# Kernel optimization log

Hardware: AMD Instinct MI355X
Metric: run time of the kernel (lower is better)

The kernel has to match this reference:

```python
import jax, jax.numpy as jnp
import numpy as np

HEADS = 8
DIM_HEAD = 32
HTK = 576
WTK = 576


def layernorm(x, g, b, eps=1e-6):
    mu = x.mean(-1, keepdims=True)
    var = ((x - mu) ** 2).mean(-1, keepdims=True)
    return (x - mu) * jax.lax.rsqrt(var + eps) * g + b


def conv2d(x, w, b, pad, groups=1):
    y = jax.lax.conv_general_dilated(
        x, w, (1, 1), [(pad, pad), (pad, pad)],
        dimension_numbers=('NCHW', 'OIHW', 'NCHW'),
        feature_group_count=groups)
    return y + b[None, :, None, None]


def prune_attn(attn, htk, wtk):
    B, H, N, _ = attn.shape
    bi = jnp.arange(B)[:, None, None]
    hi = jnp.arange(H)[None, :, None]
    # row pruning: score rows by mean over keys, keep top-k rows
    row_scores = attn.mean(-1)                       # [B,H,N]
    _, top_row = jax.lax.top_k(row_scores, htk)      # [B,H,htk]
    row_mask = jnp.zeros((B, H, N), attn.dtype).at[bi, hi, top_row].set(1.0)
    # col pruning: score cols by mean over queries, keep top-k cols
    col_scores = attn.mean(-2)                       # [B,H,N]
    _, top_col = jax.lax.top_k(col_scores, wtk)
    col_mask = jnp.zeros((B, H, N), attn.dtype).at[bi, hi, top_col].set(1.0)
    return attn * row_mask[..., :, None] * col_mask[..., None, :]


def setup_inputs() -> dict:
    key = jax.random.key(0)
    ks = jax.random.split(key, 24)
    C = 256
    hid = C * 4
    g = C // 8
    s = 0.02
    inp = {
        'x': jax.random.normal(ks[0], (2, C, 48, 48), jnp.float32),
        'qkv_w': jax.random.normal(ks[1], (C, 3 * C), jnp.float32) * s,
        'out_w': jax.random.normal(ks[2], (C, C), jnp.float32) * s,
        'ln1_g': jnp.ones((C,), jnp.float32),
        'ln1_b': jnp.zeros((C,), jnp.float32),
        'ln2_g': jnp.ones((C,), jnp.float32),
        'ln2_b': jnp.zeros((C,), jnp.float32),
        'dw_w': jax.random.normal(ks[3], (C, 1, 3, 3), jnp.float32) * s,
        'dw_b': jnp.zeros((C,), jnp.float32),
        'pw_w': jax.random.normal(ks[4], (C, C, 1, 1), jnp.float32) * s,
        'pw_b': jnp.zeros((C,), jnp.float32),
        'sg1_w': jax.random.normal(ks[5], (g, C, 1, 1), jnp.float32) * s,
        'sg1_b': jnp.zeros((g,), jnp.float32),
        'sg2_w': jax.random.normal(ks[6], (1, g, 7, 7), jnp.float32) * s,
        'sg2_b': jnp.zeros((1,), jnp.float32),
        'cg1_w': jax.random.normal(ks[7], (g, C, 1, 1), jnp.float32) * s,
        'cg1_b': jnp.zeros((g,), jnp.float32),
        'cg2_w': jax.random.normal(ks[8], (C, g, 1, 1), jnp.float32) * s,
        'cg2_b': jnp.zeros((C,), jnp.float32),
        'ff_w1': jax.random.normal(ks[9], (C, hid), jnp.float32) * s,
        'ff_b1': jnp.zeros((hid,), jnp.float32),
        'ff_w2': jax.random.normal(ks[10], (hid, C), jnp.float32) * s,
        'ff_b2': jnp.zeros((C,), jnp.float32),
        'gamma1': jnp.full((1,), 0.5, jnp.float32),
        'gamma2': jnp.full((1,), 0.5, jnp.float32),
    }
    return inp


def reference(x, qkv_w, out_w, ln1_g, ln1_b, ln2_g, ln2_b, dw_w, dw_b,
              pw_w, pw_b, sg1_w, sg1_b, sg2_w, sg2_b, cg1_w, cg1_b,
              cg2_w, cg2_b, ff_w1, ff_b1, ff_w2, ff_b2, gamma1, gamma2):
    B, C, H, W = x.shape
    N = H * W
    # ---- dual-pruned self-attention branch ----
    xa = x.transpose(0, 2, 3, 1).reshape(B, N, C)
    xa = layernorm(xa, ln1_g, ln1_b)
    qkv = xa @ qkv_w                                    # [B,N,3C]
    q, k, v = jnp.split(qkv, 3, axis=-1)
    rs = lambda t: t.reshape(B, N, HEADS, DIM_HEAD).transpose(0, 2, 1, 3)
    q, k, v = rs(q), rs(k), rs(v)                       # [B,h,N,d]
    attn = jnp.einsum('bhid,bhjd->bhij', q, k) * (DIM_HEAD ** -0.5)
    attn = prune_attn(attn, HTK, WTK)
    attn = jax.nn.softmax(attn, axis=-1)
    o = jnp.einsum('bhij,bhjd->bhid', attn, v)
    o = o.transpose(0, 2, 1, 3).reshape(B, N, C) @ out_w
    x_attn = o.reshape(B, H, W, C).transpose(0, 3, 1, 2)
    # ---- conv branch ----
    xc = conv2d(x, dw_w, dw_b, pad=1, groups=C)
    xc = conv2d(xc, pw_w, pw_b, pad=0)
    xs = x_attn + xc
    # ---- gates ----
    sg = jax.nn.silu(conv2d(xs, sg1_w, sg1_b, pad=0))
    sg = jax.nn.sigmoid(conv2d(sg, sg2_w, sg2_b, pad=3))   # [B,1,H,W]
    cg = xs.mean(axis=(2, 3), keepdims=True)                # [B,C,1,1]
    cg = jax.nn.silu(conv2d(cg, cg1_w, cg1_b, pad=0))
    cg = jax.nn.sigmoid(conv2d(cg, cg2_w, cg2_b, pad=0))
    x2 = x + gamma1[0] * (xs * sg * cg)
    # ---- FFN ----
    normed = layernorm(x2.transpose(0, 2, 3, 1), ln2_g, ln2_b)
    h = jax.nn.gelu(normed @ ff_w1 + ff_b1, approximate=False)
    ff = (h @ ff_w2 + ff_b2).transpose(0, 3, 1, 2)
    return x2 + gamma2[0] * ff
```

## Files before the change

kernel.cpp:

```cpp
#include <hip/hip_runtime.h>
#include <math.h>

#define N_PIX 2304
#define CCH   256
#define BHN   16
#define KTOP  576
#define NROWS 4608

typedef unsigned short u16;
typedef __attribute__((ext_vector_type(8))) short short8v;
typedef __attribute__((ext_vector_type(4))) float floatx4;

__device__ __forceinline__ u16 f2b(float f) {
  unsigned int u = __float_as_uint(f);
  return (u16)((u + 0x7fffu + ((u >> 16) & 1u)) >> 16);
}
__device__ __forceinline__ float b2f(u16 v) {
  return __uint_as_float(((unsigned int)v) << 16);
}

__device__ __forceinline__ void async16(const void* g, void* l) {
  __builtin_amdgcn_global_load_lds(
      (const __attribute__((address_space(1))) unsigned int*)g,
      (__attribute__((address_space(3))) unsigned int*)l, 16, 0, 0);
}

__global__ __launch_bounds__(256) void ln1t_kernel(
    const float* __restrict__ x, u16* __restrict__ xa_bf, float* __restrict__ xnhwc,
    const float* __restrict__ g, const float* __restrict__ beta)
{
  __shared__ float tile[32 * 257];
  __shared__ float redS[8 * 32], redQ[8 * 32];
  __shared__ float mu_s[32], rs_s[32];
  int tid = threadIdx.x;
  int p0g = blockIdx.x * 32;
  int bb = p0g / N_PIX; int p0 = p0g - bb * N_PIX;
  int px = tid & 31, csub = tid >> 5;
  float sacc = 0.f, qacc = 0.f;
#pragma unroll 4
  for (int it = 0; it < 32; ++it) {
    int c = it * 8 + csub;
    float v = x[((long)bb * 256 + c) * N_PIX + p0 + px];
    tile[px * 257 + c] = v;
    sacc += v; qacc += v * v;
  }
  redS[csub * 32 + px] = sacc; redQ[csub * 32 + px] = qacc;
  __syncthreads();
  if (tid < 32) {
    float s = 0.f, qq = 0.f;
#pragma unroll
    for (int j = 0; j < 8; ++j) { s += redS[j * 32 + tid]; qq += redQ[j * 32 + tid]; }
    float mu = s * (1.f / 256.f);
    float var = qq * (1.f / 256.f) - mu * mu;
    mu_s[tid] = mu; rs_s[tid] = rsqrtf(var + 1e-6f);
  }
  __syncthreads();
  float gv = g[tid], bv = beta[tid];
#pragma unroll 4
  for (int it = 0; it < 32; ++it) {
    float v = tile[it * 257 + tid];
    long orow = (long)(p0g + it) * 256 + tid;
    xnhwc[orow] = v;
    xa_bf[orow] = f2b((v - mu_s[it]) * rs_s[it] * gv + bv);
  }
}

__global__ __launch_bounds__(256) void cast_all_kernel(
    const float* __restrict__ qkv_w, const float* __restrict__ out_w,
    const float* __restrict__ pw_w, const float* __restrict__ ff_w1,
    const float* __restrict__ ff_w2, const float* __restrict__ sg1_w,
    u16* __restrict__ qkvBT, u16* __restrict__ outBT, u16* __restrict__ pwBT,
    u16* __restrict__ ff1BT, u16* __restrict__ ff2BT, u16* __restrict__ sg1BT)
{
  int i = blockIdx.x * 256 + threadIdx.x;
  if (i < 196608) { int k = i / 768, n = i - k * 768; qkvBT[n * 256 + k] = f2b(qkv_w[i]); return; }
  i -= 196608;
  if (i < 65536) { int k = i >> 8, n = i & 255; outBT[n * 256 + k] = f2b(out_w[i]); return; }
  i -= 65536;
  if (i < 65536) { pwBT[i] = f2b(pw_w[i]); return; }
  i -= 65536;
  if (i < 262144) { int k = i >> 10, n = i & 1023; ff1BT[n * 256 + k] = f2b(ff_w1[i]); return; }
  i -= 262144;
  if (i < 262144) { int k = i & 1023, n = i >> 10; ff2BT[i] = f2b(ff_w2[k * 256 + n]); return; }
  i -= 262144;
  if (i < 16384) sg1BT[i] = (i < 8192) ? f2b(sg1_w[i]) : (u16)0;
}

template<int MT, int EPI, int CS>
__global__ __launch_bounds__(256) void mgemm(
    const u16* __restrict__ A, const u16* __restrict__ BT,
    float* __restrict__ C, u16* __restrict__ C2,
    int K, int ldc, int nvalid,
    const float* __restrict__ bias, const float* __restrict__ add,
    const float* __restrict__ gamma,
    float* __restrict__ cs_out, int cs_ld)
{
  __shared__ u16 Als[MT * 64 * 32];
  __shared__ u16 Bls[64 * 32];
  int tid = threadIdx.x;
  int w = tid >> 6, lane = tid & 63;
  int row0 = blockIdx.y * (MT * 64), col0 = blockIdx.x * 64;
  const u16* Abase = A + (long)row0 * K;
  const u16* Bbase = BT + (long)col0 * K;
  int q = lane >> 4, l15 = lane & 15;

  floatx4 acc[MT][4];
#pragma unroll
  for (int mi = 0; mi < MT; ++mi)
#pragma unroll
    for (int ni = 0; ni < 4; ++ni) acc[mi][ni] = (floatx4)0.f;

  int ccB = w * 64 + lane;
  int rB = ccB >> 2, kB = (ccB & 3) << 3;

  for (int k0 = 0; k0 < K; k0 += 32) {
#pragma unroll
    for (int i = 0; i < MT; ++i) {
      int cc = w * (64 * MT) + i * 64 + lane;
      async16(Abase + (long)(cc >> 2) * K + k0 + ((cc & 3) << 3), &Als[cc * 8]);
    }
    async16(Bbase + (long)rB * K + k0 + kB, &Bls[ccB * 8]);
    __syncthreads();
    short8v a[MT];
#pragma unroll
    for (int mi = 0; mi < MT; ++mi)
      a[mi] = *(const short8v*)&Als[(w * (16 * MT) + mi * 16 + l15) * 32 + q * 8];
#pragma unroll
    for (int ni = 0; ni < 4; ++ni) {
      short8v b = *(const short8v*)&Bls[(ni * 16 + l15) * 32 + q * 8];
#pragma unroll
      for (int mi = 0; mi < MT; ++mi)
        acc[mi][ni] = __builtin_amdgcn_mfma_f32_16x16x32_bf16(a[mi], b, acc[mi][ni], 0, 0, 0);
    }
    __syncthreads();
  }

  float g2 = (EPI == 5) ? gamma[0] : 0.f;
  float cp[4] = {0.f, 0.f, 0.f, 0.f};
#pragma unroll
  for (int mi = 0; mi < MT; ++mi) {
#pragma unroll
    for (int ni = 0; ni < 4; ++ni) {
      int c = col0 + ni * 16 + l15;
      int rbase = row0 + w * (16 * MT) + mi * 16 + q * 4;
#pragma unroll
      for (int reg = 0; reg < 4; ++reg) {
        long row = rbase + reg;
        float v = acc[mi][ni][reg];
        if (EPI == 0) {
          C[row * ldc + c] = v;
          if (CS) cp[ni] += v;
        } else if (EPI == 3) {
          if (c < nvalid) {
            float t = v + bias[c];
            C[row * (long)nvalid + c] = t / (1.f + expf(-t));
          }
        } else if (EPI == 4) {
          float t = v + bias[c];
          t = 0.5f * t * (1.f + erff(t * 0.70710678118654752f));
          C2[row * ldc + c] = f2b(t);
        } else if (EPI == 5) {
          float t = add[row * 256 + c] + g2 * (v + bias[c]);
          int bb = (int)(row / N_PIX); int p = (int)(row - (long)bb * N_PIX);
          C[((long)bb * 256 + c) * N_PIX + p] = t;
        } else if (EPI == 6) {
          float t = v + bias[c] + add[row * ldc + c];
          C2[row * ldc + c] = f2b(t);
          if (CS) cp[ni] += t;
        }
      }
    }
  }
  if (CS) {
    int bb = (row0 >= N_PIX) ? 1 : 0;
#pragma unroll
    for (int ni = 0; ni < 4; ++ni) {
      float r = cp[ni];
      r += __shfl_xor(r, 16);
      r += __shfl_xor(r, 32);
      if (lane < 16) atomicAdd(&cs_out[bb * cs_ld + col0 + ni * 16 + l15], r);
    }
  }
}

__global__ __launch_bounds__(256) void topkscore_kernel(
    const float* __restrict__ qkv, const float* __restrict__ csum, int* __restrict__ out_idx)
{
  int bh = blockIdx.x, which = blockIdx.y;
  int b = bh >> 3, h = bh & 7;
  int* out = out_idx + (which * BHN + bh) * KTOP;
  __shared__ unsigned int u[N_PIX];
  __shared__ unsigned int hist[256];
  __shared__ unsigned int wtmp[4];
  __shared__ unsigned int sh_selbin, sh_selS;
  __shared__ unsigned int cnt_eq[4], cnt_sel[4];
  __shared__ float svl[32];
  int tid = threadIdx.x;
  int wave = tid >> 6, lane = tid & 63;
  unsigned long long ltmask = (1ull << lane) - 1ull;
  if (tid < 32) svl[tid] = csum[b * 768 + (which ? 0 : 256) + h * 32 + tid];
  __syncthreads();
  int off = (which ? 256 : 0) + h * 32;
  for (int i = tid; i < N_PIX; i += 256) {
    const float4* p4 = (const float4*)(qkv + ((long)(b * N_PIX + i)) * 768 + off);
    float sc = 0.f;
#pragma unroll
    for (int j = 0; j < 8; ++j) {
      float4 v = p4[j];
      sc += v.x * svl[j * 4] + v.y * svl[j * 4 + 1] + v.z * svl[j * 4 + 2] + v.w * svl[j * 4 + 3];
    }
    unsigned int bu = __float_as_uint(sc);
    u[i] = (bu & 0x80000000u) ? ~bu : (bu | 0x80000000u);
  }
  __syncthreads();
  unsigned int prefix = 0u, kRem = KTOP;
  for (int pass = 0; pass < 4; ++pass) {
    int shift = 24 - pass * 8;
    hist[tid] = 0u;
    __syncthreads();
    unsigned int mask = (pass == 0) ? 0u : (0xFFFFFFFFu << (shift + 8));
    for (int i = tid; i < N_PIX; i += 256) {
      unsigned int v = u[i];
      if ((v & mask) == prefix) atomicAdd(&hist[(v >> shift) & 255u], 1u);
    }
    __syncthreads();
    int v = (int)hist[255 - tid];
    int xsc = v;
#pragma unroll
    for (int o = 1; o < 64; o <<= 1) { int y = __shfl_up(xsc, o); if (lane >= o) xsc += y; }
    if (lane == 63) wtmp[wave] = (unsigned int)xsc;
    __syncthreads();
    int wadd = 0;
    for (int ww = 0; ww < wave; ++ww) wadd += (int)wtmp[ww];
    unsigned int S = (unsigned int)(xsc + wadd - v);
    if (S < kRem && S + (unsigned int)v >= kRem) { sh_selbin = (unsigned int)(255 - tid); sh_selS = S; }
    __syncthreads();
    prefix |= (sh_selbin << shift);
    kRem -= sh_selS;
    __syncthreads();
  }
  unsigned int T = prefix;
  unsigned int run_sel = 0u, run_eq = 0u;
  for (int c0 = 0; c0 < N_PIX; c0 += 256) {
    int i = c0 + tid;
    unsigned int v = u[i];
    bool isGt = v > T, isEq = (v == T);
    unsigned long long be = __ballot(isEq);
    unsigned int eqpre = (unsigned int)__popcll(be & ltmask);
    if (lane == 0) cnt_eq[wave] = (unsigned int)__popcll(be);
    __syncthreads();
    unsigned int eqoff = run_eq + eqpre;
    for (int ww = 0; ww < wave; ++ww) eqoff += cnt_eq[ww];
    bool selF = isGt || (isEq && eqoff < kRem);
    unsigned long long bs = __ballot(selF);
    unsigned int spre = (unsigned int)__popcll(bs & ltmask);
    if (lane == 0) cnt_sel[wave] = (unsigned int)__popcll(bs);
    __syncthreads();
    unsigned int soff = run_sel + spre;
    for (int ww = 0; ww < wave; ++ww) soff += cnt_sel[ww];
    if (selF) out[soff] = i;
    unsigned int te = 0, ts = 0;
#pragma unroll
    for (int ww = 0; ww < 4; ++ww) { te += cnt_eq[ww]; ts += cnt_sel[ww]; }
    run_eq += te; run_sel += ts;
    __syncthreads();
  }
}

__global__ __launch_bounds__(256) void gather_kernel(
    const float* __restrict__ qkv, const int* __restrict__ idx,
    u16* __restrict__ Qg, u16* __restrict__ Kg, u16* __restrict__ VgT,
    float* __restrict__ vneg)
{
  __shared__ float red[256];
  int bh = blockIdx.y;
  int tid = threadIdx.x;
  int r = blockIdx.x * 8 + (tid >> 5);
  int d = tid & 31;
  int b = bh >> 3, h = bh & 7;
  int rn = idx[bh * KTOP + r];
  int cn = idx[(BHN + bh) * KTOP + r];
  const float scale = 0.17677669529663687f;
  float vv = qkv[((long)(b * N_PIX + cn)) * 768 + 512 + h * 32 + d];
  Qg [((long)bh * KTOP + r) * 32 + d] = f2b(qkv[((long)(b * N_PIX + rn)) * 768 + h * 32 + d] * scale);
  Kg [((long)bh * KTOP + r) * 32 + d] = f2b(qkv[((long)(b * N_PIX + cn)) * 768 + 256 + h * 32 + d]);
  VgT[((long)bh * 32 + d) * 584 + r] = f2b(vv);
  red[tid] = vv;
  __syncthreads();
  if (tid < 32) {
    float s = 0.f;
#pragma unroll
    for (int j = 0; j < 8; ++j) s += red[j * 32 + tid];
    atomicAdd(&vneg[bh * 32 + tid], s);
  }
}

__global__ __launch_bounds__(256) void ofill_kernel(
    const float* __restrict__ csum, u16* __restrict__ ofull)
{
  int c = threadIdx.x;
  int b = blockIdx.x / N_PIX;
  ofull[(long)blockIdx.x * 256 + c] = f2b(csum[b * 768 + 512 + c] * (1.f / (float)N_PIX));
}

__global__ __launch_bounds__(256) void attn_kernel(
    const u16* __restrict__ Qg, const u16* __restrict__ Kg, const u16* __restrict__ VgT,
    const float* __restrict__ csum, const float* __restrict__ vneg,
    const int* __restrict__ idx, u16* __restrict__ ofull)
{
  __shared__ u16 Pls[32 * 584];
  __shared__ float wmax[4 * 32], wsum[4 * 32];
  __shared__ float emv_s[32], invd_s[32], vdif_s[32];
  int bh = blockIdx.y;
  int row0 = blockIdx.x * 32;
  int tid = threadIdx.x;
  int w = tid >> 6, lane = tid & 63;
  int q = lane >> 4, l15 = lane & 15;
  int b = bh >> 3, h = bh & 7;
  if (tid < 32) vdif_s[tid] = csum[b * 768 + 512 + h * 32 + tid] - vneg[bh * 32 + tid];
  const u16* Qb = Qg + (long)bh * KTOP * 32;
  const u16* Kb = Kg + (long)bh * KTOP * 32;
  short8v af[2];
#pragma unroll
  for (int mi = 0; mi < 2; ++mi)
    af[mi] = *(const short8v*)(Qb + ((long)(row0 + mi * 16 + l15)) * 32 + q * 8);
  floatx4 sacc[2][9];
#pragma unroll
  for (int mi = 0; mi < 2; ++mi)
#pragma unroll
    for (int ni = 0; ni < 9; ++ni) sacc[mi][ni] = (floatx4)0.f;
#pragma unroll
  for (int ni = 0; ni < 9; ++ni) {
    int n = w * 144 + ni * 16 + l15;
    short8v bf = *(const short8v*)(Kb + (long)n * 32 + q * 8);
#pragma unroll
    for (int mi = 0; mi < 2; ++mi)
      sacc[mi][ni] = __builtin_amdgcn_mfma_f32_16x16x32_bf16(af[mi], bf, sacc[mi][ni], 0, 0, 0);
  }
#pragma unroll
  for (int mi = 0; mi < 2; ++mi)
#pragma unroll
    for (int reg = 0; reg < 4; ++reg) {
      float m = sacc[mi][0][reg];
#pragma unroll
      for (int ni = 1; ni < 9; ++ni) m = fmaxf(m, sacc[mi][ni][reg]);
#pragma unroll
      for (int o = 1; o < 16; o <<= 1) m = fmaxf(m, __shfl_xor(m, o));
      if (l15 == 0) wmax[w * 32 + mi * 16 + q * 4 + reg] = m;
    }
  __syncthreads();
#pragma unroll
  for (int mi = 0; mi < 2; ++mi)
#pragma unroll
    for (int reg = 0; reg < 4; ++reg) {
      int r = mi * 16 + q * 4 + reg;
      float gm = fmaxf(fmaxf(fmaxf(wmax[r], wmax[32 + r]), fmaxf(wmax[64 + r], wmax[96 + r])), 0.f);
      float s = 0.f;
#pragma unroll
      for (int ni = 0; ni < 9; ++ni) {
        float e = expf(sacc[mi][ni][reg] - gm);
        s += e;
        Pls[r * 584 + w * 144 + ni * 16 + l15] = f2b(e);
      }
#pragma unroll
      for (int o = 1; o < 16; o <<= 1) s += __shfl_xor(s, o);
      if (l15 == 0) wsum[w * 32 + r] = s;
    }
  __syncthreads();
  if (tid < 32) {
    float gm = fmaxf(fmaxf(fmaxf(wmax[tid], wmax[32 + tid]), fmaxf(wmax[64 + tid], wmax[96 + tid])), 0.f);
    float s = wsum[tid] + wsum[32 + tid] + wsum[64 + tid] + wsum[96 + tid];
    float em = expf(-gm);
    float inv = 1.f / (s + (float)(N_PIX - KTOP) * em);
    invd_s[tid] = inv;
    emv_s[tid] = em * inv;
  }
  __syncthreads();
  int mw = w & 1, nw = w >> 1;
  const u16* Vb = VgT + (long)bh * 32 * 584;
  floatx4 acc = (floatx4)0.f;
#pragma unroll
  for (int kt = 0; kt < 18; ++kt) {
    int k0 = kt * 32;
    short8v a = *(const short8v*)&Pls[(mw * 16 + l15) * 584 + k0 + q * 8];
    short8v bb = *(const short8v*)(Vb + (long)(nw * 16 + l15) * 584 + k0 + q * 8);
    acc = __builtin_amdgcn_mfma_f32_16x16x32_bf16(a, bb, acc, 0, 0, 0);
  }
  int d = nw * 16 + l15;
  float vd = vdif_s[d];
#pragma unroll
  for (int reg = 0; reg < 4; ++reg) {
    int r = mw * 16 + q * 4 + reg;
    float o = acc[reg] * invd_s[r] + emv_s[r] * vd;
    int n = idx[bh * KTOP + row0 + r];
    ofull[((long)(b * N_PIX + n)) * 256 + h * 32 + d] = f2b(o);
  }
}

__global__ __launch_bounds__(256) void dwconv_kernel(
    const float* __restrict__ xnhwc, const float* __restrict__ w,
    const float* __restrict__ bias, u16* __restrict__ out_nhwc)
{
  int pix = blockIdx.x;
  int b = pix / N_PIX; int p = pix - b * N_PIX;
  int y = p / 48, xx = p - y * 48;
  int c = threadIdx.x;
  float acc = bias[c];
#pragma unroll
  for (int ky = 0; ky < 3; ++ky) {
    int yy = y + ky - 1; if (yy < 0 || yy >= 48) continue;
#pragma unroll
    for (int kx = 0; kx < 3; ++kx) {
      int xc = xx + kx - 1; if (xc < 0 || xc >= 48) continue;
      acc += w[c * 9 + ky * 3 + kx] * xnhwc[((long)(b * N_PIX + yy * 48 + xc)) * 256 + c];
    }
  }
  out_nhwc[(long)pix * 256 + c] = f2b(acc);
}

__global__ __launch_bounds__(256) void sg2_kernel(
    const float* __restrict__ sga, const float* __restrict__ w,
    const float* __restrict__ b1, float* __restrict__ sgate)
{
  __shared__ float ws[32 * 49];
  __shared__ float red[4 * 64];
  int by = blockIdx.x; int b = by / 48, y = by - b * 48;
  int t = threadIdx.x;
  for (int i = t; i < 32 * 49; i += 256) ws[i] = w[i];
  __syncthreads();
  int xx = t & 63, gg = t >> 6;
  float acc = 0.f;
  if (xx < 48) {
    for (int ky = 0; ky < 7; ++ky) {
      int yy = y + ky - 3; if (yy < 0 || yy >= 48) continue;
      for (int kx = 0; kx < 7; ++kx) {
        int xc = xx + kx - 3; if (xc < 0 || xc >= 48) continue;
        const float4* sp = (const float4*)(sga + ((long)(b * N_PIX + yy * 48 + xc)) * 32 + gg * 8);
        float4 v0 = sp[0], v1 = sp[1];
        int wb = gg * 8 * 49 + ky * 7 + kx;
        acc += ws[wb] * v0.x + ws[wb + 49] * v0.y + ws[wb + 98] * v0.z + ws[wb + 147] * v0.w;
        acc += ws[wb + 196] * v1.x + ws[wb + 245] * v1.y + ws[wb + 294] * v1.z + ws[wb + 343] * v1.w;
      }
    }
  }
  red[gg * 64 + xx] = acc;
  __syncthreads();
  if (t < 48) {
    float tot = b1[0] + red[t] + red[64 + t] + red[128 + t] + red[192 + t];
    sgate[b * N_PIX + y * 48 + t] = 1.f / (1.f + expf(-tot));
  }
}

__global__ __launch_bounds__(256) void cgmlp_kernel(
    const float* __restrict__ cgm, const float* __restrict__ w1, const float* __restrict__ b1,
    const float* __restrict__ w2, const float* __restrict__ b2, float* __restrict__ cgate)
{
  int b = blockIdx.x; int t = threadIdx.x;
  __shared__ float m[256];
  __shared__ float a[32];
  m[t] = cgm[b * 256 + t] * (1.f / (float)N_PIX);
  __syncthreads();
  if (t < 32) {
    float s = b1[t];
    for (int c = 0; c < 256; ++c) s += w1[t * 256 + c] * m[c];
    a[t] = s / (1.f + expf(-s));
  }
  __syncthreads();
  float s = b2[t];
#pragma unroll
  for (int g = 0; g < 32; ++g) s += w2[t * 32 + g] * a[g];
  cgate[b * 256 + t] = 1.f / (1.f + expf(-s));
}

__global__ __launch_bounds__(256) void x2ln_kernel(
    const float* __restrict__ xnhwc, const u16* __restrict__ xs_bf,
    const float* __restrict__ sgate, const float* __restrict__ cgate,
    const float* __restrict__ gamma1, float* __restrict__ x2,
    const float* __restrict__ g, const float* __restrict__ bvec, u16* __restrict__ normed)
{
  __shared__ float red[256];
  int pix = blockIdx.x; int b = pix / N_PIX;
  int c = threadIdx.x;
  float xsv = b2f(xs_bf[(long)pix * 256 + c]);
  float v = xnhwc[(long)pix * 256 + c] + gamma1[0] * xsv * sgate[pix] * cgate[b * 256 + c];
  x2[(long)pix * 256 + c] = v;
  red[c] = v; __syncthreads();
  for (int off = 128; off > 0; off >>= 1) { if (c < off) red[c] += red[c + off]; __syncthreads(); }
  float mu = red[0] * (1.f / 256.f);
  __syncthreads();
  float dv = v - mu;
  red[c] = dv * dv; __syncthreads();
  for (int off = 128; off > 0; off >>= 1) { if (c < off) red[c] += red[c + off]; __syncthreads(); }
  float var = red[0] * (1.f / 256.f);
  normed[(long)pix * 256 + c] = f2b(dv * rsqrtf(var + 1e-6f) * g[c] + bvec[c]);
}

extern "C" void kernel_launch(void* const* d_in, const int* in_sizes, int n_in,
                              void* d_out, int out_size, void* d_ws, size_t ws_size,
                              hipStream_t stream) {
  (void)in_sizes; (void)n_in; (void)out_size; (void)ws_size;
  const float* x      = (const float*)d_in[0];
  const float* qkv_w  = (const float*)d_in[1];
  const float* out_w  = (const float*)d_in[2];
  const float* ln1_g  = (const float*)d_in[3];
  const float* ln1_b  = (const float*)d_in[4];
  const float* ln2_g  = (const float*)d_in[5];
  const float* ln2_b  = (const float*)d_in[6];
  const float* dw_w   = (const float*)d_in[7];
  const float* dw_b   = (const float*)d_in[8];
  const float* pw_w   = (const float*)d_in[9];
  const float* pw_b   = (const float*)d_in[10];
  const float* sg1_w  = (const float*)d_in[11];
  const float* sg1_b  = (const float*)d_in[12];
  const float* sg2_w  = (const float*)d_in[13];
  const float* sg2_b  = (const float*)d_in[14];
  const float* cg1_w  = (const float*)d_in[15];
  const float* cg1_b  = (const float*)d_in[16];
  const float* cg2_w  = (const float*)d_in[17];
  const float* cg2_b  = (const float*)d_in[18];
  const float* ff_w1  = (const float*)d_in[19];
  const float* ff_b1  = (const float*)d_in[20];
  const float* ff_w2  = (const float*)d_in[21];
  const float* ff_b2  = (const float*)d_in[22];
  const float* gamma1 = (const float*)d_in[23];
  const float* gamma2 = (const float*)d_in[24];
  float* out = (float*)d_out;
  float* ws  = (float*)d_ws;

  float* qkv     = ws + 0;
  float* attn_out= ws + 3538944;
  float* x2      = ws + 4718592;
  float* xnhwc   = ws + 5898240;
  u16*   ofull_bf= (u16*)(ws + 7077888);
  u16*   xa_bf   = (u16*)(ws + 7667712);
  u16*   xs_bf   = (u16*)(ws + 8257536);
  u16*   Qg_bf   = (u16*)(ws + 8847360);
  u16*   Kg_bf   = (u16*)(ws + 8994816);
  u16*   VgT     = (u16*)(ws + 9142272);
  float* sga     = ws + 9291776;
  float* csum    = ws + 9439232;
  float* vneg    = ws + 9440768;
  float* cgm     = ws + 9441280;
  float* sgate   = ws + 9441792;
  float* cgate   = ws + 9446400;
  int*   idxb    = (int*)(ws + 9446912);
  u16*   qkvBT   = (u16*)(ws + 9465344);
  u16*   outBT   = (u16*)(ws + 9563648);
  u16*   pwBT    = (u16*)(ws + 9596416);
  u16*   ff1BT   = (u16*)(ws + 9629184);
  u16*   ff2BT   = (u16*)(ws + 9760256);
  u16*   sg1BT   = (u16*)(ws + 9891328);
  u16*   h_bf     = (u16*)qkv;
  u16*   normed_bf= (u16*)(ws + 2359296);
  u16*   dwc_bf   = xa_bf;

  dim3 blk(256);
  hipMemsetAsync(csum, 0, 2560 * sizeof(float), stream);

  cast_all_kernel<<<dim3(3392), blk, 0, stream>>>(qkv_w, out_w, pw_w, ff_w1, ff_w2, sg1_w,
      qkvBT, outBT, pwBT, ff1BT, ff2BT, sg1BT);

  ln1t_kernel<<<dim3(144), blk, 0, stream>>>(x, xa_bf, xnhwc, ln1_g, ln1_b);
  mgemm<2, 0, 1><<<dim3(12, 36), blk, 0, stream>>>(xa_bf, qkvBT, qkv, nullptr,
      256, 768, 768, nullptr, nullptr, nullptr, csum, 768);
  topkscore_kernel<<<dim3(BHN, 2), blk, 0, stream>>>(qkv, csum, idxb);
  gather_kernel<<<dim3(72, BHN), blk, 0, stream>>>(qkv, idxb, Qg_bf, Kg_bf, VgT, vneg);
  ofill_kernel<<<dim3(NROWS), blk, 0, stream>>>(csum, ofull_bf);
  attn_kernel<<<dim3(18, BHN), blk, 0, stream>>>(Qg_bf, Kg_bf, VgT, csum, vneg, idxb, ofull_bf);
  mgemm<1, 0, 0><<<dim3(4, 72), blk, 0, stream>>>(ofull_bf, outBT, attn_out, nullptr,
      256, 256, 256, nullptr, nullptr, nullptr, nullptr, 0);

  dwconv_kernel<<<dim3(NROWS), blk, 0, stream>>>(xnhwc, dw_w, dw_b, dwc_bf);
  mgemm<1, 6, 1><<<dim3(4, 72), blk, 0, stream>>>(dwc_bf, pwBT, nullptr, xs_bf,
      256, 256, 256, pw_b, attn_out, nullptr, cgm, 256);

  mgemm<1, 3, 0><<<dim3(1, 72), blk, 0, stream>>>(xs_bf, sg1BT, sga, nullptr,
      256, 32, 32, sg1_b, nullptr, nullptr, nullptr, 0);
  sg2_kernel<<<dim3(96), blk, 0, stream>>>(sga, sg2_w, sg2_b, sgate);
  cgmlp_kernel<<<dim3(2), blk, 0, stream>>>(cgm, cg1_w, cg1_b, cg2_w, cg2_b, cgate);

  x2ln_kernel<<<dim3(NROWS), blk, 0, stream>>>(xnhwc, xs_bf, sgate, cgate, gamma1, x2,
      ln2_g, ln2_b, normed_bf);

  mgemm<2, 4, 0><<<dim3(16, 36), blk, 0, stream>>>(normed_bf, ff1BT, nullptr, h_bf,
      256, 1024, 1024, ff_b1, nullptr, nullptr, nullptr, 0);
  mgemm<1, 5, 0><<<dim3(4, 72), blk, 0, stream>>>(h_bf, ff2BT, out, nullptr,
      1024, 256, 256, ff_b2, x2, gamma2, nullptr, 0);
}
```

Before: 269.8 us.

## Merge small kernels, widen GEMM N-tiles, recompute x2 in FFN2 epilogue

Folds the weight-cast kernel into the first layernorm kernel, the ofill kernel into gather, and the channel-gate MLP into the spatial-gate kernel, cutting kernel launches. The GEMM template gains an N-tile multiplier, and the QKV, FFN1 and FFN2 GEMMs use 128-wide column tiles for more reuse per block, with fewer blocks in exchange. The x2 buffer is no longer stored. The FFN2 epilogue recomputes it from xnhwc, xs, sgate and cgate, trading a full fp32 write and read for extra gathers in the epilogue.

Measured after the change: 291.2 us. 1.08x slower.

```diff
diff --git a/kernel.cpp b/kernel.cpp
--- a/kernel.cpp
+++ b/kernel.cpp
@@ -25,14 +25,34 @@
       (__attribute__((address_space(3))) unsigned int*)l, 16, 0, 0);
 }
 
-__global__ __launch_bounds__(256) void ln1t_kernel(
+__global__ __launch_bounds__(256) void lncast_kernel(
     const float* __restrict__ x, u16* __restrict__ xa_bf, float* __restrict__ xnhwc,
-    const float* __restrict__ g, const float* __restrict__ beta)
+    const float* __restrict__ g, const float* __restrict__ beta,
+    const float* __restrict__ qkv_w, const float* __restrict__ out_w,
+    const float* __restrict__ pw_w, const float* __restrict__ ff_w1,
+    const float* __restrict__ ff_w2, const float* __restrict__ sg1_w,
+    u16* __restrict__ qkvBT, u16* __restrict__ outBT, u16* __restrict__ pwBT,
+    u16* __restrict__ ff1BT, u16* __restrict__ ff2BT, u16* __restrict__ sg1BT)
 {
   __shared__ float tile[32 * 257];
   __shared__ float redS[8 * 32], redQ[8 * 32];
   __shared__ float mu_s[32], rs_s[32];
   int tid = threadIdx.x;
+  if (blockIdx.x >= 144) {
+    int i = (blockIdx.x - 144) * 256 + tid;
+    if (i < 196608) { int k = i / 768, n = i - k * 768; qkvBT[n * 256 + k] = f2b(qkv_w[i]); return; }
+    i -= 196608;
+    if (i < 65536) { int k = i >> 8, n = i & 255; outBT[n * 256 + k] = f2b(out_w[i]); return; }
+    i -= 65536;
+    if (i < 65536) { pwBT[i] = f2b(pw_w[i]); return; }
+    i -= 65536;
+    if (i < 262144) { int k = i >> 10, n = i & 1023; ff1BT[n * 256 + k] = f2b(ff_w1[i]); return; }
+    i -= 262144;
+    if (i < 262144) { int k = i & 1023, n = i >> 10; ff2BT[i] = f2b(ff_w2[k * 256 + n]); return; }
+    i -= 262144;
+    if (i < 16384) sg1BT[i] = (i < 8192) ? f2b(sg1_w[i]) : (u16)0;
+    return;
+  }
   int p0g = blockIdx.x * 32;
   int bb = p0g / N_PIX; int p0 = p0g - bb * N_PIX;
   int px = tid & 31, csub = tid >> 5;
@@ -65,53 +85,31 @@
   }
 }
 
-__global__ __launch_bounds__(256) void cast_all_kernel(
-    const float* __restrict__ qkv_w, const float* __restrict__ out_w,
-    const float* __restrict__ pw_w, const float* __restrict__ ff_w1,
-    const float* __restrict__ ff_w2, const float* __restrict__ sg1_w,
-    u16* __restrict__ qkvBT, u16* __restrict__ outBT, u16* __restrict__ pwBT,
-    u16* __restrict__ ff1BT, u16* __restrict__ ff2BT, u16* __restrict__ sg1BT)
-{
-  int i = blockIdx.x * 256 + threadIdx.x;
-  if (i < 196608) { int k = i / 768, n = i - k * 768; qkvBT[n * 256 + k] = f2b(qkv_w[i]); return; }
-  i -= 196608;
-  if (i < 65536) { int k = i >> 8, n = i & 255; outBT[n * 256 + k] = f2b(out_w[i]); return; }
-  i -= 65536;
-  if (i < 65536) { pwBT[i] = f2b(pw_w[i]); return; }
-  i -= 65536;
-  if (i < 262144) { int k = i >> 10, n = i & 1023; ff1BT[n * 256 + k] = f2b(ff_w1[i]); return; }
-  i -= 262144;
-  if (i < 262144) { int k = i & 1023, n = i >> 10; ff2BT[i] = f2b(ff_w2[k * 256 + n]); return; }
-  i -= 262144;
-  if (i < 16384) sg1BT[i] = (i < 8192) ? f2b(sg1_w[i]) : (u16)0;
-}
-
-template<int MT, int EPI, int CS>
+template<int MT, int NT, int EPI, int CS>
 __global__ __launch_bounds__(256) void mgemm(
     const u16* __restrict__ A, const u16* __restrict__ BT,
     float* __restrict__ C, u16* __restrict__ C2,
     int K, int ldc, int nvalid,
     const float* __restrict__ bias, const float* __restrict__ add,
     const float* __restrict__ gamma,
-    float* __restrict__ cs_out, int cs_ld)
+    float* __restrict__ cs_out, int cs_ld,
+    const u16* __restrict__ xs2, const float* __restrict__ sgv,
+    const float* __restrict__ cgv, const float* __restrict__ g1p)
 {
   __shared__ u16 Als[MT * 64 * 32];
-  __shared__ u16 Bls[64 * 32];
+  __shared__ u16 Bls[NT * 64 * 32];
   int tid = threadIdx.x;
   int w = tid >> 6, lane = tid & 63;
-  int row0 = blockIdx.y * (MT * 64), col0 = blockIdx.x * 64;
+  int row0 = blockIdx.y * (MT * 64), col0 = blockIdx.x * (NT * 64);
   const u16* Abase = A + (long)row0 * K;
   const u16* Bbase = BT + (long)col0 * K;
   int q = lane >> 4, l15 = lane & 15;
 
-  floatx4 acc[MT][4];
+  floatx4 acc[MT][4 * NT];
 #pragma unroll
   for (int mi = 0; mi < MT; ++mi)
 #pragma unroll
-    for (int ni = 0; ni < 4; ++ni) acc[mi][ni] = (floatx4)0.f;
-
-  int ccB = w * 64 + lane;
-  int rB = ccB >> 2, kB = (ccB & 3) << 3;
+    for (int ni = 0; ni < 4 * NT; ++ni) acc[mi][ni] = (floatx4)0.f;
 
   for (int k0 = 0; k0 < K; k0 += 32) {
 #pragma unroll
@@ -119,14 +117,18 @@
       int cc = w * (64 * MT) + i * 64 + lane;
       async16(Abase + (long)(cc >> 2) * K + k0 + ((cc & 3) << 3), &Als[cc * 8]);
     }
-    async16(Bbase + (long)rB * K + k0 + kB, &Bls[ccB * 8]);
+#pragma unroll
+    for (int j = 0; j < NT; ++j) {
+      int cc = w * (64 * NT) + j * 64 + lane;
+      async16(Bbase + (long)(cc >> 2) * K + k0 + ((cc & 3) << 3), &Bls[cc * 8]);
+    }
     __syncthreads();
     short8v a[MT];
 #pragma unroll
     for (int mi = 0; mi < MT; ++mi)
       a[mi] = *(const short8v*)&Als[(w * (16 * MT) + mi * 16 + l15) * 32 + q * 8];
 #pragma unroll
-    for (int ni = 0; ni < 4; ++ni) {
+    for (int ni = 0; ni < 4 * NT; ++ni) {
       short8v b = *(const short8v*)&Bls[(ni * 16 + l15) * 32 + q * 8];
 #pragma unroll
       for (int mi = 0; mi < MT; ++mi)
@@ -136,11 +138,14 @@
   }
 
   float g2 = (EPI == 5) ? gamma[0] : 0.f;
-  float cp[4] = {0.f, 0.f, 0.f, 0.f};
+  float g1v = (EPI == 5) ? g1p[0] : 0.f;
+  float cp[4 * NT];
+#pragma unroll
+  for (int ni = 0; ni < 4 * NT; ++ni) cp[ni] = 0.f;
 #pragma unroll
   for (int mi = 0; mi < MT; ++mi) {
 #pragma unroll
-    for (int ni = 0; ni < 4; ++ni) {
+    for (int ni = 0; ni < 4 * NT; ++ni) {
       int c = col0 + ni * 16 + l15;
       int rbase = row0 + w * (16 * MT) + mi * 16 + q * 4;
 #pragma unroll
@@ -160,8 +165,10 @@
           t = 0.5f * t * (1.f + erff(t * 0.70710678118654752f));
           C2[row * ldc + c] = f2b(t);
         } else if (EPI == 5) {
-          float t = add[row * 256 + c] + g2 * (v + bias[c]);
           int bb = (int)(row / N_PIX); int p = (int)(row - (long)bb * N_PIX);
+          float xsv = b2f(xs2[row * 256 + c]);
+          float x2v = add[row * 256 + c] + g1v * xsv * sgv[row] * cgv[bb * 256 + c];
+          float t = x2v + g2 * (v + bias[c]);
           C[((long)bb * 256 + c) * N_PIX + p] = t;
         } else if (EPI == 6) {
           float t = v + bias[c] + add[row * ldc + c];
@@ -174,7 +181,7 @@
   if (CS) {
     int bb = (row0 >= N_PIX) ? 1 : 0;
 #pragma unroll
-    for (int ni = 0; ni < 4; ++ni) {
+    for (int ni = 0; ni < 4 * NT; ++ni) {
       float r = cp[ni];
       r += __shfl_xor(r, 16);
       r += __shfl_xor(r, 32);
@@ -270,7 +277,7 @@
 __global__ __launch_bounds__(256) void gather_kernel(
     const float* __restrict__ qkv, const int* __restrict__ idx,
     u16* __restrict__ Qg, u16* __restrict__ Kg, u16* __restrict__ VgT,
-    float* __restrict__ vneg)
+    float* __restrict__ vneg, const float* __restrict__ csum, u16* __restrict__ ofull)
 {
   __shared__ float red[256];
   int bh = blockIdx.y;
@@ -286,6 +293,17 @@
   Kg [((long)bh * KTOP + r) * 32 + d] = f2b(qkv[((long)(b * N_PIX + cn)) * 768 + 256 + h * 32 + d]);
   VgT[((long)bh * 32 + d) * 584 + r] = f2b(vv);
   red[tid] = vv;
+  int bid = blockIdx.y * 72 + blockIdx.x;
+  int row = 4 * bid + (tid >> 6);
+  int b2 = row / N_PIX;
+  int c4 = (tid & 63) * 4;
+  const float* vm = csum + b2 * 768 + 512 + c4;
+  ushort4 ov;
+  ov.x = f2b(vm[0] * (1.f / (float)N_PIX));
+  ov.y = f2b(vm[1] * (1.f / (float)N_PIX));
+  ov.z = f2b(vm[2] * (1.f / (float)N_PIX));
+  ov.w = f2b(vm[3] * (1.f / (float)N_PIX));
+  *(ushort4*)&ofull[(long)row * 256 + c4] = ov;
   __syncthreads();
   if (tid < 32) {
     float s = 0.f;
@@ -293,14 +311,6 @@
     for (int j = 0; j < 8; ++j) s += red[j * 32 + tid];
     atomicAdd(&vneg[bh * 32 + tid], s);
   }
-}
-
-__global__ __launch_bounds__(256) void ofill_kernel(
-    const float* __restrict__ csum, u16* __restrict__ ofull)
-{
-  int c = threadIdx.x;
-  int b = blockIdx.x / N_PIX;
-  ofull[(long)blockIdx.x * 256 + c] = f2b(csum[b * 768 + 512 + c] * (1.f / (float)N_PIX));
 }
 
 __global__ __launch_bounds__(256) void attn_kernel(
@@ -418,14 +428,34 @@
   out_nhwc[(long)pix * 256 + c] = f2b(acc);
 }
 
-__global__ __launch_bounds__(256) void sg2_kernel(
+__global__ __launch_bounds__(256) void sgcg_kernel(
     const float* __restrict__ sga, const float* __restrict__ w,
-    const float* __restrict__ b1, float* __restrict__ sgate)
+    const float* __restrict__ b1, float* __restrict__ sgate,
+    const float* __restrict__ cgm, const float* __restrict__ cw1, const float* __restrict__ cb1,
+    const float* __restrict__ cw2, const float* __restrict__ cb2, float* __restrict__ cgate)
 {
   __shared__ float ws[32 * 49];
   __shared__ float red[4 * 64];
+  __shared__ float m[256];
+  __shared__ float a[32];
+  int t = threadIdx.x;
+  if (blockIdx.x >= 96) {
+    int b = blockIdx.x - 96;
+    m[t] = cgm[b * 256 + t] * (1.f / (float)N_PIX);
+    __syncthreads();
+    if (t < 32) {
+      float s = cb1[t];
+      for (int c = 0; c < 256; ++c) s += cw1[t * 256 + c] * m[c];
+      a[t] = s / (1.f + expf(-s));
+    }
+    __syncthreads();
+    float s = cb2[t];
+#pragma unroll
+    for (int g = 0; g < 32; ++g) s += cw2[t * 32 + g] * a[g];
+    cgate[b * 256 + t] = 1.f / (1.f + expf(-s));
+    return;
+  }
   int by = blockIdx.x; int b = by / 48, y = by - b * 48;
-  int t = threadIdx.x;
   for (int i = t; i < 32 * 49; i += 256) ws[i] = w[i];
   __syncthreads();
   int xx = t & 63, gg = t >> 6;
@@ -451,31 +481,10 @@
   }
 }
 
-__global__ __launch_bounds__(256) void cgmlp_kernel(
-    const float* __restrict__ cgm, const float* __restrict__ w1, const float* __restrict__ b1,
-    const float* __restrict__ w2, const float* __restrict__ b2, float* __restrict__ cgate)
-{
-  int b = blockIdx.x; int t = threadIdx.x;
-  __shared__ float m[256];
-  __shared__ float a[32];
-  m[t] = cgm[b * 256 + t] * (1.f / (float)N_PIX);
-  __syncthreads();
-  if (t < 32) {
-    float s = b1[t];
-    for (int c = 0; c < 256; ++c) s += w1[t * 256 + c] * m[c];
-    a[t] = s / (1.f + expf(-s));
-  }
-  __syncthreads();
-  float s = b2[t];
-#pragma unroll
-  for (int g = 0; g < 32; ++g) s += w2[t * 32 + g] * a[g];
-  cgate[b * 256 + t] = 1.f / (1.f + expf(-s));
-}
-
-__global__ __launch_bounds__(256) void x2ln_kernel(
+__global__ __launch_bounds__(256) void gln_kernel(
     const float* __restrict__ xnhwc, const u16* __restrict__ xs_bf,
     const float* __restrict__ sgate, const float* __restrict__ cgate,
-    const float* __restrict__ gamma1, float* __restrict__ x2,
+    const float* __restrict__ gamma1,
     const float* __restrict__ g, const float* __restrict__ bvec, u16* __restrict__ normed)
 {
   __shared__ float red[256];
@@ -483,7 +492,6 @@
   int c = threadIdx.x;
   float xsv = b2f(xs_bf[(long)pix * 256 + c]);
   float v = xnhwc[(long)pix * 256 + c] + gamma1[0] * xsv * sgate[pix] * cgate[b * 256 + c];
-  x2[(long)pix * 256 + c] = v;
   red[c] = v; __syncthreads();
   for (int off = 128; off > 0; off >>= 1) { if (c < off) red[c] += red[c + off]; __syncthreads(); }
   float mu = red[0] * (1.f / 256.f);
@@ -529,27 +537,26 @@
 
   float* qkv     = ws + 0;
   float* attn_out= ws + 3538944;
-  float* x2      = ws + 4718592;
-  float* xnhwc   = ws + 5898240;
-  u16*   ofull_bf= (u16*)(ws + 7077888);
-  u16*   xa_bf   = (u16*)(ws + 7667712);
-  u16*   xs_bf   = (u16*)(ws + 8257536);
-  u16*   Qg_bf   = (u16*)(ws + 8847360);
-  u16*   Kg_bf   = (u16*)(ws + 8994816);
-  u16*   VgT     = (u16*)(ws + 9142272);
-  float* sga     = ws + 9291776;
-  float* csum    = ws + 9439232;
-  float* vneg    = ws + 9440768;
-  float* cgm     = ws + 9441280;
-  float* sgate   = ws + 9441792;
-  float* cgate   = ws + 9446400;
-  int*   idxb    = (int*)(ws + 9446912);
-  u16*   qkvBT   = (u16*)(ws + 9465344);
-  u16*   outBT   = (u16*)(ws + 9563648);
-  u16*   pwBT    = (u16*)(ws + 9596416);
-  u16*   ff1BT   = (u16*)(ws + 9629184);
-  u16*   ff2BT   = (u16*)(ws + 9760256);
-  u16*   sg1BT   = (u16*)(ws + 9891328);
+  float* xnhwc   = ws + 4718592;
+  u16*   ofull_bf= (u16*)(ws + 5898240);
+  u16*   xa_bf   = (u16*)(ws + 6488064);
+  u16*   xs_bf   = (u16*)(ws + 7077888);
+  u16*   Qg_bf   = (u16*)(ws + 7667712);
+  u16*   Kg_bf   = (u16*)(ws + 7815168);
+  u16*   VgT     = (u16*)(ws + 7962624);
+  float* sga     = ws + 8112128;
+  float* csum    = ws + 8259584;
+  float* vneg    = ws + 8261120;
+  float* cgm     = ws + 8261632;
+  float* sgate   = ws + 8262144;
+  float* cgate   = ws + 8266752;
+  int*   idxb    = (int*)(ws + 8267264);
+  u16*   qkvBT   = (u16*)(ws + 8285696);
+  u16*   outBT   = (u16*)(ws + 8384000);
+  u16*   pwBT    = (u16*)(ws + 8416768);
+  u16*   ff1BT   = (u16*)(ws + 8449536);
+  u16*   ff2BT   = (u16*)(ws + 8580608);
+  u16*   sg1BT   = (u16*)(ws + 8711680);
   u16*   h_bf     = (u16*)qkv;
   u16*   normed_bf= (u16*)(ws + 2359296);
   u16*   dwc_bf   = xa_bf;
@@ -557,33 +564,33 @@
   dim3 blk(256);
   hipMemsetAsync(csum, 0, 2560 * sizeof(float), stream);
 
-  cast_all_kernel<<<dim3(3392), blk, 0, stream>>>(qkv_w, out_w, pw_w, ff_w1, ff_w2, sg1_w,
+  lncast_kernel<<<dim3(3536), blk, 0, stream>>>(x, xa_bf, xnhwc, ln1_g, ln1_b,
+      qkv_w, out_w, pw_w, ff_w1, ff_w2, sg1_w,
       qkvBT, outBT, pwBT, ff1BT, ff2BT, sg1BT);
 
-  ln1t_kernel<<<dim3(144), blk, 0, stream>>>(x, xa_bf, xnhwc, ln1_g, ln1_b);
-  mgemm<2, 0, 1><<<dim3(12, 36), blk, 0, stream>>>(xa_bf, qkvBT, qkv, nullptr,
-      256, 768, 768, nullptr, nullptr, nullptr, csum, 768);
+  mgemm<2, 2, 0, 1><<<dim3(6, 36), blk, 0, stream>>>(xa_bf, qkvBT, qkv, nullptr,
+      256, 768, 768, nullptr, nullptr, nullptr, csum, 768, nullptr, nullptr, nullptr, nullptr);
   topkscore_kernel<<<dim3(BHN, 2), blk, 0, stream>>>(qkv, csum, idxb);
-  gather_kernel<<<dim3(72, BHN), blk, 0, stream>>>(qkv, idxb, Qg_bf, Kg_bf, VgT, vneg);
-  ofill_kernel<<<dim3(NROWS), blk, 0, stream>>>(csum, ofull_bf);
+  gather_kernel<<<dim3(72, BHN), blk, 0, stream>>>(qkv, idxb, Qg_bf, Kg_bf, VgT, vneg,
+      csum, ofull_bf);
   attn_kernel<<<dim3(18, BHN), blk, 0, stream>>>(Qg_bf, Kg_bf, VgT, csum, vneg, idxb, ofull_bf);
-  mgemm<1, 0, 0><<<dim3(4, 72), blk, 0, stream>>>(ofull_bf, outBT, attn_out, nullptr,
-      256, 256, 256, nullptr, nullptr, nullptr, nullptr, 0);
+  mgemm<1, 1, 0, 0><<<dim3(4, 72), blk, 0, stream>>>(ofull_bf, outBT, attn_out, nullptr,
+      256, 256, 256, nullptr, nullptr, nullptr, nullptr, 0, nullptr, nullptr, nullptr, nullptr);
 
   dwconv_kernel<<<dim3(NROWS), blk, 0, stream>>>(xnhwc, dw_w, dw_b, dwc_bf);
-  mgemm<1, 6, 1><<<dim3(4, 72), blk, 0, stream>>>(dwc_bf, pwBT, nullptr, xs_bf,
-      256, 256, 256, pw_b, attn_out, nullptr, cgm, 256);
-
-  mgemm<1, 3, 0><<<dim3(1, 72), blk, 0, stream>>>(xs_bf, sg1BT, sga, nullptr,
-      256, 32, 32, sg1_b, nullptr, nullptr, nullptr, 0);
-  sg2_kernel<<<dim3(96), blk, 0, stream>>>(sga, sg2_w, sg2_b, sgate);
-  cgmlp_kernel<<<dim3(2), blk, 0, stream>>>(cgm, cg1_w, cg1_b, cg2_w, cg2_b, cgate);
-
-  x2ln_kernel<<<dim3(NROWS), blk, 0, stream>>>(xnhwc, xs_bf, sgate, cgate, gamma1, x2,
+  mgemm<1, 1, 6, 1><<<dim3(4, 72), blk, 0, stream>>>(dwc_bf, pwBT, nullptr, xs_bf,
+      256, 256, 256, pw_b, attn_out, nullptr, cgm, 256, nullptr, nullptr, nullptr, nullptr);
+
+  mgemm<1, 1, 3, 0><<<dim3(1, 72), blk, 0, stream>>>(xs_bf, sg1BT, sga, nullptr,
+      256, 32, 32, sg1_b, nullptr, nullptr, nullptr, 0, nullptr, nullptr, nullptr, nullptr);
+  sgcg_kernel<<<dim3(98), blk, 0, stream>>>(sga, sg2_w, sg2_b, sgate,
+      cgm, cg1_w, cg1_b, cg2_w, cg2_b, cgate);
+
+  gln_kernel<<<dim3(NROWS), blk, 0, stream>>>(xnhwc, xs_bf, sgate, cgate, gamma1,
       ln2_g, ln2_b, normed_bf);
 
-  mgemm<2, 4, 0><<<dim3(16, 36), blk, 0, stream>>>(normed_bf, ff1BT, nullptr, h_bf,
-      256, 1024, 1024, ff_b1, nullptr, nullptr, nullptr, 0);
-  mgemm<1, 5, 0><<<dim3(4, 72), blk, 0, stream>>>(h_bf, ff2BT, out, nullptr,
-      1024, 256, 256, ff_b2, x2, gamma2, nullptr, 0);
-}
+  mgemm<2, 2, 4, 0><<<dim3(8, 36), blk, 0, stream>>>(normed_bf, ff1BT, nullptr, h_bf,
+      256, 1024, 1024, ff_b1, nullptr, nullptr, nullptr, 0, nullptr, nullptr, nullptr, nullptr);
+  mgemm<1, 2, 5, 0><<<dim3(2, 72), blk, 0, stream>>>(h_bf, ff2BT, out, nullptr,
+      1024, 256, 256, ff_b2, xnhwc, gamma2, nullptr, 0, xs_bf, sgate, cgate, gamma1);
+}
```
